# Optimization experiments

Measured on AMD Instinct MI355X. Metric: run time of the kernel, lower is better.

Reference implementation:

```python
import jax, jax.numpy as jnp
import numpy as np
from jax import lax

BN_EPS = 1e-5
B, C_IN, HW = 512, 3, 128  # crop batch, channels, crop size
C1, C2 = 32, 64
DIST_THRESHOLD = 0.55


def setup_inputs() -> dict:
    key = jax.random.key(0)
    ks = jax.random.split(key, 13)
    return {
        "crops": jax.random.normal(ks[0], (B, C_IN, HW, HW), jnp.float32),
        "w1": jax.random.normal(ks[1], (C1, C_IN, 3, 3), jnp.float32) * 0.1,
        "b1": jax.random.normal(ks[2], (C1,), jnp.float32) * 0.1,
        "g1": jax.random.uniform(ks[3], (C1,), jnp.float32),
        "be1": jax.random.normal(ks[4], (C1,), jnp.float32) * 0.1,
        "m1": jax.random.normal(ks[5], (C1,), jnp.float32) * 0.1,
        "v1": jax.random.uniform(ks[6], (C1,), jnp.float32),
        "w2": jax.random.normal(ks[7], (C2, C1, 3, 3), jnp.float32) * 0.05,
        "b2": jax.random.normal(ks[8], (C2,), jnp.float32) * 0.1,
        "g2": jax.random.uniform(ks[9], (C2,), jnp.float32),
        "be2": jax.random.normal(ks[10], (C2,), jnp.float32) * 0.1,
        "m2": jax.random.normal(ks[11], (C2,), jnp.float32) * 0.1,
        "v2": jax.random.uniform(ks[12], (C2,), jnp.float32),
    }


def _conv(x, w, b, stride):
    y = lax.conv_general_dilated(
        x, w, window_strides=(stride, stride), padding=((1, 1), (1, 1)),
        dimension_numbers=("NCHW", "OIHW", "NCHW"))
    return y + b[None, :, None, None]


def _bn(x, gamma, beta, mean, var):
    inv = gamma * lax.rsqrt(var + BN_EPS)
    return x * inv[None, :, None, None] + (beta - mean * inv)[None, :, None, None]


def _maxpool2(x):
    return lax.reduce_window(x, -jnp.inf, lax.max, (1, 1, 2, 2), (1, 1, 2, 2), "VALID")


def reference(crops, w1, b1, g1, be1, m1, v1, w2, b2, g2, be2, m2, v2):
    # layer1: Conv(3->32, s1, p1) + BN + ReLU + MaxPool2  -> [B, 32, 64, 64]
    h = _maxpool2(jax.nn.relu(_bn(_conv(crops, w1, b1, 1), g1, be1, m1, v1)))
    # layer2: Conv(32->64, s2, p1) + BN + Sigmoid + MaxPool2 -> [B, 64, 16, 16]
    feat = _maxpool2(jax.nn.sigmoid(_bn(_conv(h, w2, b2, 2), g2, be2, m2, v2)))
    # per-crop distribution score thresholded as in uniqueDistribution/MLE
    scores = feat.mean(axis=(1, 2, 3))            # [B]
    detected = scores >= DIST_THRESHOLD           # [B] bool
    return feat, scores, detected
```

## Files before the change

kernel.cpp:

```cpp
#include <hip/hip_runtime.h>
#include <math.h>

#define BN_EPS 1e-5f
#define HW_ 128

typedef unsigned short u16_t;
typedef unsigned int u32_t;

typedef __bf16 bf16x8 __attribute__((ext_vector_type(8)));
typedef float f32x4 __attribute__((ext_vector_type(4)));
typedef float f32x16 __attribute__((ext_vector_type(16)));
typedef u32_t u32x4 __attribute__((ext_vector_type(4)));
typedef u32x4 u32x4_ma __attribute__((may_alias));
typedef u16_t u16_ma __attribute__((may_alias));

static __device__ __forceinline__ u16_t f2bf(float f) {
    u32_t u = __float_as_uint(f);
    return (u16_t)((u + 0x7FFFu + ((u >> 16) & 1u)) >> 16);
}
static __device__ __forceinline__ u32_t packbf(float a, float b) {
    return (u32_t)f2bf(a) | ((u32_t)f2bf(b) << 16);
}
static __device__ __forceinline__ bf16x8 ld_frag16(const u16_t* p) {
    union { u32x4 u; bf16x8 f; } x;
    x.u = *(const u32x4_ma*)p;
    return x.f;
}
static __device__ __forceinline__ bf16x8 ld_frag32(const u32_t* p) {
    union { u32x4 u; bf16x8 f; } x;
    x.u = *(const u32x4_ma*)p;
    return x.f;
}
static __device__ __forceinline__ bf16x8 asbf(u32x4 u) {
    union { u32x4 u; bf16x8 f; } x;
    x.u = u;
    return x.f;
}

#define WSUM_OFF 0
#define W2R_OFF  512
#define WF_OFF   9728
#define PT_OFF   11008
#define BN1_OFF  12192
#define BN2_OFF  12256
#define WS_TOTAL 12384

#define CI_PITCH 304
#define CI_U32   (36 * 152)

__global__ __launch_bounds__(512) void prep_kernel(
    const float* __restrict__ w1, const float* __restrict__ b1,
    const float* __restrict__ g1, const float* __restrict__ be1,
    const float* __restrict__ m1, const float* __restrict__ v1,
    const float* __restrict__ w2, const float* __restrict__ b2,
    const float* __restrict__ g2, const float* __restrict__ be2,
    const float* __restrict__ m2, const float* __restrict__ v2,
    u32_t* __restrict__ ws)
{
    const int tid = threadIdx.x;
    ws[WSUM_OFF + tid] = 0u;

    for (int idx = tid; idx < 9216; idx += 512) {
        int H   = idx / 4608;
        int rem = idx - H * 4608;
        int tap = rem >> 9;
        int r2  = rem & 511;
        int ocl = r2 >> 4;
        int icp = r2 & 15;
        const float* wp = w2 + (H * 32 + ocl) * 288 + tap;
        ws[W2R_OFF + idx] = packbf(wp[(2 * icp) * 9], wp[(2 * icp + 1) * 9]);
    }
    if (tid < 320) {
        int s = tid >> 6, lane = tid & 63;
        int n32 = lane & 31, halfk = lane >> 5;
        int p = 2 * s + halfk;
        bool valid = (p <= 8);
        const float* wp = w1 + n32 * 27 + (valid ? p : 8);
        float wa = valid ? wp[0]  : 0.f;
        float wb = valid ? wp[9]  : 0.f;
        float wc = valid ? wp[18] : 0.f;
        u32x4 f;
        f[0] = packbf(wa, wb); f[1] = packbf(wc, 0.f); f[2] = 0u; f[3] = 0u;
        ((u32x4_ma*)(ws + WF_OFF))[tid] = f;
    }
    for (int idx = tid; idx < 1184; idx += 512) {
        int tt = idx >> 5, n32 = idx & 31;
        int gA = n32 >> 2, sub = n32 & 3;
        int pA = tt * 8 + gA;
        int gy = (pA * 241) >> 12; gy = min(gy, 16);
        int gx = min(pA - gy * 17, 16);
        int cy = 2 * gy + (sub >> 1), cx = 2 * gx + (sub & 1);
        ws[PT_OFF + idx] = (u32_t)(cy * CI_PITCH + cx * 8);
    }
    if (tid < 32) {
        float inv = g1[tid] * rsqrtf(v1[tid] + BN_EPS);
        float sh  = b1[tid] * inv + be1[tid] - m1[tid] * inv;
        ws[BN1_OFF + 2 * tid]     = __float_as_uint(inv);
        ws[BN1_OFF + 2 * tid + 1] = __float_as_uint(sh);
    }
    if (tid >= 64 && tid < 128) {
        int ch = tid - 64;
        float inv = g2[ch] * rsqrtf(v2[ch] + BN_EPS);
        float sh  = b2[ch] * inv + be2[ch] - m2[ch] * inv;
        ws[BN2_OFF + 2 * ch]     = __float_as_uint(inv);
        ws[BN2_OFF + 2 * ch + 1] = __float_as_uint(sh);
    }
}

__global__ __launch_bounds__(512, 8) void fused_cnn_kernel(
    const float* __restrict__ crops, const u32_t* __restrict__ tab,
    float* __restrict__ out, float* __restrict__ wsum)
{
    __shared__ __align__(16) u32_t uniS[CI_U32];
    __shared__ __align__(16) u16_t hS[289 * 32];
    __shared__ float bn2S[128];
    __shared__ float redS[8];

    const int tid  = threadIdx.x;
    const int wave = tid >> 6;
    const int lane = tid & 63;
    const int quad = lane >> 4;
    const int r    = lane & 15;
    const int n32  = lane & 31;
    const int halfk = lane >> 5;

    const int blk = blockIdx.x;
    const int img = blk >> 4;
    const int t   = blk & 15;
    const int fy0 = (t >> 2) * 4;
    const int fx0 = (t & 3) * 4;
    const int crop_y0 = 8 * fy0 - 3;
    const int crop_x0 = 8 * fx0 - 3;
    const bool interior = (fy0 != 0) && (fx0 != 0);

    if (tid < 128) bn2S[tid] = __uint_as_float(tab[BN2_OFF + tid]);
    const float* cbase = crops + (size_t)img * (3 * HW_ * HW_);
    #pragma unroll
    for (int i = 0; i < 3; ++i) {
        int idx = tid + 512 * i;
        if (idx < 1296) {
            int rr = (idx * 1821) >> 16;
            int cc = idx - rr * 36;
            int gr = crop_y0 + rr, gc = crop_x0 + cc;
            float v0 = 0.f, v1v = 0.f, v2v = 0.f;
            if (gr >= 0 && gr < HW_ && gc >= 0 && gc < HW_) {
                const float* p = cbase + gr * HW_ + gc;
                v0  = p[0];
                v1v = p[HW_ * HW_];
                v2v = p[2 * HW_ * HW_];
            }
            u32x4 w;
            w[0] = packbf(v0, v1v); w[1] = packbf(v2v, 0.f); w[2] = 0u; w[3] = 0u;
            *(u32x4_ma*)&uniS[rr * 152 + cc * 4] = w;
        }
    }

    u32x4 wf[5];
    const u32x4_ma* wft = (const u32x4_ma*)(tab + WF_OFF);
    #pragma unroll
    for (int s = 0; s < 5; ++s) wf[s] = wft[s * 64 + lane];
    const float inv1 = __uint_as_float(tab[BN1_OFF + 2 * n32]);
    const float sh1  = __uint_as_float(tab[BN1_OFF + 2 * n32 + 1]);
    __syncthreads();

    const int off0 = halfk ? 8          : 0;
    const int off1 = halfk ? 304        : 16;
    const int off2 = halfk ? 304 + 16   : 304 + 8;
    const int off3 = halfk ? 608 + 8    : 608;
    const int off4 = 608 + 16;
    const u16_t* cropsI = (const u16_t*)uniS;

    #pragma unroll 1
    for (int tt = wave; tt < 37; tt += 8) {
        const u16_t* base = cropsI + tab[PT_OFF + tt * 32 + n32];

        bf16x8 a0 = ld_frag16(base + off0);
        bf16x8 a1 = ld_frag16(base + off1);
        bf16x8 a2 = ld_frag16(base + off2);
        bf16x8 a3 = ld_frag16(base + off3);
        bf16x8 a4 = ld_frag16(base + off4);

        f32x16 acc = {0.f,0.f,0.f,0.f,0.f,0.f,0.f,0.f,
                      0.f,0.f,0.f,0.f,0.f,0.f,0.f,0.f};
        acc = __builtin_amdgcn_mfma_f32_32x32x16_bf16(a0, asbf(wf[0]), acc, 0, 0, 0);
        acc = __builtin_amdgcn_mfma_f32_32x32x16_bf16(a1, asbf(wf[1]), acc, 0, 0, 0);
        acc = __builtin_amdgcn_mfma_f32_32x32x16_bf16(a2, asbf(wf[2]), acc, 0, 0, 0);
        acc = __builtin_amdgcn_mfma_f32_32x32x16_bf16(a3, asbf(wf[3]), acc, 0, 0, 0);
        acc = __builtin_amdgcn_mfma_f32_32x32x16_bf16(a4, asbf(wf[4]), acc, 0, 0, 0);

        #pragma unroll
        for (int q = 0; q < 4; ++q) {
            int pD = tt * 8 + 2 * q + halfk;
            float m4 = fmaxf(fmaxf(acc[4 * q], acc[4 * q + 1]),
                             fmaxf(acc[4 * q + 2], acc[4 * q + 3]));
            float val = fmaxf(fmaf(m4, inv1, sh1), 0.f);
            if (!interior) {
                int gyD = (pD * 241) >> 12;
                int gxD = pD - gyD * 17;
                int y2 = 4 * fy0 - 1 + gyD, x2 = 4 * fx0 - 1 + gxD;
                if (y2 < 0 || y2 > 63 || x2 < 0 || x2 > 63) val = 0.f;
            }
            if (pD < 289) hS[pD * 32 + n32] = f2bf(val);
        }
    }
    __syncthreads();

    float* outp = out + (size_t)img * 16384;
    const f32x4 zero4 = {0.f, 0.f, 0.f, 0.f};
    float ssum = 0.f;
    #pragma unroll 1
    for (int H = 0; H < 2; ++H) {
        const u32x4_ma* w2t = (const u32x4_ma*)(tab + W2R_OFF + H * 4608);
        u32x4_ma* uni4 = (u32x4_ma*)uniS;
        for (int i = tid; i < 1152; i += 512) uni4[i] = w2t[i];
        __syncthreads();

        const int mt  = wave & 1;
        const int nt0 = wave >> 1;
        const int rhi = r >> 3, rlo = r & 7;
        f32x4 acc = zero4;
        #pragma unroll
        for (int s = 0; s < 9; ++s) {
            const int ky = s / 3, kx = s - 3 * (s / 3);
            bf16x8 af = ld_frag32(&uniS[(s * 32 + mt * 16 + r) * 16 + quad * 4]);
            int hrow = 4 * nt0 + 2 * rhi + ky;
            int hcol = 2 * rlo + kx;
            bf16x8 bx = ld_frag16(&hS[(hrow * 17 + hcol) * 32 + quad * 8]);
            acc = __builtin_amdgcn_mfma_f32_16x16x32_bf16(af, bx, acc, 0, 0, 0);
        }
        const bool active = ((r & 9) == 0);
        const int fxl = r >> 1;
        const int fy  = fy0 + nt0;
        #pragma unroll
        for (int reg = 0; reg < 4; ++reg) {
            int oc = H * 32 + mt * 16 + quad * 4 + reg;
            float v = acc[reg];
            float m = fmaxf(v, __shfl_xor(v, 1));
            m = fmaxf(m, __shfl_xor(m, 8));
            float z = fmaf(m, bn2S[oc * 2], bn2S[oc * 2 + 1]);
            float sig = 1.f / (1.f + expf(-z));
            if (active) {
                outp[oc * 256 + fy * 16 + fx0 + fxl] = sig;
                ssum += sig;
            }
        }
        if (H == 0) __syncthreads();
    }

    #pragma unroll
    for (int off = 32; off > 0; off >>= 1)
        ssum += __shfl_xor(ssum, off);
    if (lane == 0) redS[wave] = ssum;
    __syncthreads();
    if (tid == 0) {
        float bs = 0.f;
        #pragma unroll
        for (int w = 0; w < 8; ++w) bs += redS[w];
        atomicAdd(&wsum[img], bs);
    }
}

__global__ void finalize_kernel(const float* __restrict__ ws,
                                float* __restrict__ scores,
                                float* __restrict__ detected) {
    int i = threadIdx.x;
    float mean = ws[i] * (1.f / 16384.f);
    scores[i] = mean;
    detected[i] = (mean >= 0.55f) ? 1.f : 0.f;
}

extern "C" void kernel_launch(void* const* d_in, const int* in_sizes, int n_in,
                              void* d_out, int out_size, void* d_ws, size_t ws_size,
                              hipStream_t stream) {
    (void)in_sizes; (void)n_in; (void)out_size; (void)ws_size;
    const float* crops = (const float*)d_in[0];
    const float* w1  = (const float*)d_in[1];
    const float* b1  = (const float*)d_in[2];
    const float* g1  = (const float*)d_in[3];
    const float* be1 = (const float*)d_in[4];
    const float* m1  = (const float*)d_in[5];
    const float* v1  = (const float*)d_in[6];
    const float* w2  = (const float*)d_in[7];
    const float* b2  = (const float*)d_in[8];
    const float* g2  = (const float*)d_in[9];
    const float* be2 = (const float*)d_in[10];
    const float* m2  = (const float*)d_in[11];
    const float* v2  = (const float*)d_in[12];
    float* out = (float*)d_out;
    u32_t* ws  = (u32_t*)d_ws;

    prep_kernel<<<1, 512, 0, stream>>>(
        w1, b1, g1, be1, m1, v1, w2, b2, g2, be2, m2, v2, ws);
    fused_cnn_kernel<<<8192, 512, 0, stream>>>(
        crops, ws, out, (float*)ws);
    finalize_kernel<<<1, 512, 0, stream>>>(
        (const float*)ws, out + 8388608, out + 8388608 + 512);
}
```

Baseline: 309.7 us.

## Swap conv2 MFMA operands, swizzle hS layout, read weights from global

```diff
diff --git a/kernel.cpp b/kernel.cpp
--- a/kernel.cpp
+++ b/kernel.cpp
@@ -41,9 +41,9 @@
 #define W2R_OFF  512
 #define WF_OFF   9728
 #define PT_OFF   11008
-#define BN1_OFF  12192
-#define BN2_OFF  12256
-#define WS_TOTAL 12384
+#define BN1_OFF  12288
+#define BN2_OFF  12352
+#define WS_TOTAL 12480
 
 #define CI_PITCH 304
 #define CI_U32   (36 * 152)
@@ -83,12 +83,12 @@
         f[0] = packbf(wa, wb); f[1] = packbf(wc, 0.f); f[2] = 0u; f[3] = 0u;
         ((u32x4_ma*)(ws + WF_OFF))[tid] = f;
     }
-    for (int idx = tid; idx < 1184; idx += 512) {
+    for (int idx = tid; idx < 1280; idx += 512) {
         int tt = idx >> 5, n32 = idx & 31;
         int gA = n32 >> 2, sub = n32 & 3;
         int pA = tt * 8 + gA;
         int gy = (pA * 241) >> 12; gy = min(gy, 16);
-        int gx = min(pA - gy * 17, 16);
+        int gx = min(pA - gy * 17, 16); gx = max(gx, 0);
         int cy = 2 * gy + (sub >> 1), cx = 2 * gx + (sub & 1);
         ws[PT_OFF + idx] = (u32_t)(cy * CI_PITCH + cx * 8);
     }
@@ -113,7 +113,6 @@
 {
     __shared__ __align__(16) u32_t uniS[CI_U32];
     __shared__ __align__(16) u16_t hS[289 * 32];
-    __shared__ float bn2S[128];
     __shared__ float redS[8];
 
     const int tid  = threadIdx.x;
@@ -133,7 +132,6 @@
     const int crop_x0 = 8 * fx0 - 3;
     const bool interior = (fy0 != 0) && (fx0 != 0);
 
-    if (tid < 128) bn2S[tid] = __uint_as_float(tab[BN2_OFF + tid]);
     const float* cbase = crops + (size_t)img * (3 * HW_ * HW_);
     #pragma unroll
     for (int i = 0; i < 3; ++i) {
@@ -169,9 +167,12 @@
     const int off3 = halfk ? 608 + 8    : 608;
     const int off4 = 608 + 16;
     const u16_t* cropsI = (const u16_t*)uniS;
-
-    #pragma unroll 1
-    for (int tt = wave; tt < 37; tt += 8) {
+    const int hsub = n32 & 7;
+    const int hchk = n32 >> 3;
+
+    #pragma unroll
+    for (int i = 0; i < 5; ++i) {
+        int tt = wave + 8 * i;
         const u16_t* base = cropsI + tab[PT_OFF + tt * 32 + n32];
 
         bf16x8 a0 = ld_frag16(base + off0);
@@ -200,51 +201,42 @@
                 int y2 = 4 * fy0 - 1 + gyD, x2 = 4 * fx0 - 1 + gxD;
                 if (y2 < 0 || y2 > 63 || x2 < 0 || x2 > 63) val = 0.f;
             }
-            if (pD < 289) hS[pD * 32 + n32] = f2bf(val);
+            if (pD < 289) {
+                int chk = hchk ^ ((pD >> 1) & 3);
+                hS[pD * 32 + chk * 8 + hsub] = f2bf(val);
+            }
         }
     }
     __syncthreads();
 
     float* outp = out + (size_t)img * 16384;
     const f32x4 zero4 = {0.f, 0.f, 0.f, 0.f};
+    const int mt  = wave & 1;
+    const int nt0 = wave >> 1;
+    const int cy2 = 2 * nt0 + ((r >> 1) & 1);
+    const int cx2 = 2 * (r >> 2) + (r & 1);
+    const int fy  = fy0 + nt0;
     float ssum = 0.f;
     #pragma unroll 1
     for (int H = 0; H < 2; ++H) {
-        const u32x4_ma* w2t = (const u32x4_ma*)(tab + W2R_OFF + H * 4608);
-        u32x4_ma* uni4 = (u32x4_ma*)uniS;
-        for (int i = tid; i < 1152; i += 512) uni4[i] = w2t[i];
-        __syncthreads();
-
-        const int mt  = wave & 1;
-        const int nt0 = wave >> 1;
-        const int rhi = r >> 3, rlo = r & 7;
+        const u32_t* wz = tab + W2R_OFF + H * 4608;
+        const int oc = H * 32 + mt * 16 + r;
+        const float s2  = __uint_as_float(tab[BN2_OFF + 2 * oc]);
+        const float sh2 = __uint_as_float(tab[BN2_OFF + 2 * oc + 1]);
         f32x4 acc = zero4;
         #pragma unroll
         for (int s = 0; s < 9; ++s) {
             const int ky = s / 3, kx = s - 3 * (s / 3);
-            bf16x8 af = ld_frag32(&uniS[(s * 32 + mt * 16 + r) * 16 + quad * 4]);
-            int hrow = 4 * nt0 + 2 * rhi + ky;
-            int hcol = 2 * rlo + kx;
-            bf16x8 bx = ld_frag16(&hS[(hrow * 17 + hcol) * 32 + quad * 8]);
-            acc = __builtin_amdgcn_mfma_f32_16x16x32_bf16(af, bx, acc, 0, 0, 0);
+            int p = (2 * cy2 + ky) * 17 + (2 * cx2 + kx);
+            bf16x8 ah = ld_frag16(&hS[p * 32 + ((quad ^ ((p >> 1) & 3)) << 3)]);
+            bf16x8 bw = ld_frag32(&wz[(s * 32 + mt * 16 + r) * 16 + quad * 4]);
+            acc = __builtin_amdgcn_mfma_f32_16x16x32_bf16(ah, bw, acc, 0, 0, 0);
         }
-        const bool active = ((r & 9) == 0);
-        const int fxl = r >> 1;
-        const int fy  = fy0 + nt0;
-        #pragma unroll
-        for (int reg = 0; reg < 4; ++reg) {
-            int oc = H * 32 + mt * 16 + quad * 4 + reg;
-            float v = acc[reg];
-            float m = fmaxf(v, __shfl_xor(v, 1));
-            m = fmaxf(m, __shfl_xor(m, 8));
-            float z = fmaf(m, bn2S[oc * 2], bn2S[oc * 2 + 1]);
-            float sig = 1.f / (1.f + expf(-z));
-            if (active) {
-                outp[oc * 256 + fy * 16 + fx0 + fxl] = sig;
-                ssum += sig;
-            }
-        }
-        if (H == 0) __syncthreads();
+        float m4 = fmaxf(fmaxf(acc[0], acc[1]), fmaxf(acc[2], acc[3]));
+        float z = fmaf(m4, s2, sh2);
+        float sig = 1.f / (1.f + expf(-z));
+        outp[oc * 256 + fy * 16 + fx0 + quad] = sig;
+        ssum += sig;
     }
 
     #pragma unroll
```

Measured after the change: 289.7 us. -6.4%, faster.
